# Performance work log

Measured on AMD Instinct MI355X. Metric: run time of the kernel, lower is better.

The kernel has to match this reference:

```python
import jax, jax.numpy as jnp
import numpy as np

B, N, C, H, NRES = 32, 1024, 384, 1024, 20
NTAB = 21  # 20 aa + unknown, per AlphaFold residue_constants


def setup_inputs() -> dict:
    key = jax.random.key(0)
    ks = jax.random.split(key, 16)
    s = 0.02
    inp = {}
    inp['act'] = jax.random.normal(ks[0], (B, N, C), jnp.float32)
    inp['angles'] = jax.random.normal(ks[1], (B, N, 7, 2), jnp.float32)
    inp['rigids'] = jax.random.normal(ks[2], (B, N, 7), jnp.float32)
    inp['fixed_mask'] = jax.random.randint(ks[3], (B, N), 0, 2, jnp.int32)
    inp['seq_t'] = jax.random.randint(ks[4], (B, N), 0, NRES, jnp.int32)
    inp['residx_atom37_to_atom14'] = jax.random.randint(ks[5], (B, N, 37), 0, 14, jnp.int32)
    inp['ln_g'] = jnp.ones((C,), jnp.float32)
    inp['ln_b'] = jnp.zeros((C,), jnp.float32)
    inp['w1'] = jax.random.normal(ks[6], (C, H), jnp.float32) * s
    inp['b1'] = jnp.zeros((H,), jnp.float32)
    inp['w2'] = jax.random.normal(ks[7], (H, H), jnp.float32) * s
    inp['b2'] = jnp.zeros((H,), jnp.float32)
    inp['w3'] = jax.random.normal(ks[8], (H, NRES), jnp.float32) * s
    inp['b3'] = jnp.zeros((NRES,), jnp.float32)
    # stand-in residue_constants tables (same shapes/dtypes as AlphaFold's)
    inp['default_frames'] = jax.random.normal(ks[9], (NTAB, 8, 4, 4), jnp.float32)
    inp['group_idx'] = jax.random.randint(ks[10], (NTAB, 14), 0, 8, jnp.int32)
    inp['atom14_mask'] = (jax.random.uniform(ks[11], (NTAB, 14)) > 0.3).astype(jnp.float32)
    inp['atom37_mask'] = (jax.random.uniform(ks[12], (NTAB, 37)) > 0.3).astype(jnp.float32)
    inp['lit_positions'] = jax.random.normal(ks[13], (NTAB, 14, 3), jnp.float32)
    return inp


def quat_to_rot(q):
    q = q / jnp.sqrt(jnp.sum(q * q, axis=-1, keepdims=True) + 1e-8)
    w, x, y, z = q[..., 0], q[..., 1], q[..., 2], q[..., 3]
    r = jnp.stack([
        1 - 2 * (y * y + z * z), 2 * (x * y - w * z), 2 * (x * z + w * y),
        2 * (x * y + w * z), 1 - 2 * (x * x + z * z), 2 * (y * z - w * x),
        2 * (x * z - w * y), 2 * (y * z + w * x), 1 - 2 * (x * x + y * y)
    ], axis=-1)
    return r.reshape(q.shape[:-1] + (3, 3))


def compose(r1, t1, r2, t2):
    # rigid composition: (r1, t1) o (r2, t2)
    return (jnp.einsum('...ij,...jk->...ik', r1, r2),
            jnp.einsum('...ij,...j->...i', r1, t2) + t1)


def reference(act, angles, rigids, fixed_mask, seq_t, residx_atom37_to_atom14,
              ln_g, ln_b, w1, b1, w2, b2, w3, b3,
              default_frames, group_idx, atom14_mask, atom37_mask, lit_positions):
    # --- small MLP head ---
    mu = jnp.mean(act, axis=-1, keepdims=True)
    var = jnp.var(act, axis=-1, keepdims=True)
    h = (act - mu) / jnp.sqrt(var + 1e-5) * ln_g + ln_b
    h = jax.nn.relu(h @ w1 + b1)
    h = jax.nn.relu(h @ w2 + b2)
    logits = h @ w3 + b3                                # [B,N,20]
    p_0t = jax.nn.softmax(logits, axis=-1)
    seq0 = jnp.argmax(p_0t, axis=-1).astype(jnp.int32)
    seq0 = seq0 * (1 - fixed_mask) + seq_t * fixed_mask  # [B,N]

    # --- backbone frame from quaternion rigids ---
    rb = quat_to_rot(rigids[..., :4])                    # [B,N,3,3]
    tb = rigids[..., 4:]                                 # [B,N,3]

    # --- torsion_angles_to_frames ---
    df = default_frames[seq0]                            # [B,N,8,4,4]
    dr, dt = df[..., :3, :3], df[..., :3, 3]
    sin, cos = angles[..., 0], angles[..., 1]            # [B,N,7]
    z1 = jnp.zeros_like(sin[..., :1])
    sin8 = jnp.concatenate([z1, sin], axis=-1)           # backbone group has angle 0
    cos8 = jnp.concatenate([jnp.ones_like(z1), cos], axis=-1)
    zz, oo = jnp.zeros_like(sin8), jnp.ones_like(sin8)
    rx = jnp.stack([oo, zz, zz, zz, cos8, -sin8, zz, sin8, cos8], axis=-1)
    rx = rx.reshape(sin8.shape + (3, 3))                 # rotation about x-axis
    fr = jnp.einsum('bngij,bngjk->bngik', dr, rx)        # frames to backbone (pre-chain)
    ft = dt
    # chain chi2->chi1, chi3->chi2, chi4->chi3
    r5, t5 = compose(fr[..., 4, :, :], ft[..., 4, :], fr[..., 5, :, :], ft[..., 5, :])
    r6, t6 = compose(r5, t5, fr[..., 6, :, :], ft[..., 6, :])
    r7, t7 = compose(r6, t6, fr[..., 7, :, :], ft[..., 7, :])
    frot = jnp.concatenate([fr[..., :5, :, :], r5[..., None, :, :], r6[..., None, :, :], r7[..., None, :, :]], axis=-3)
    ftr = jnp.concatenate([ft[..., :5, :], t5[..., None, :], t6[..., None, :], t7[..., None, :]], axis=-2)
    grot, gtr = compose(rb[..., None, :, :], tb[..., None, :], frot, ftr)  # [B,N,8,3,3],[B,N,8,3]

    # --- frames_and_literature_positions_to_atom14_pos ---
    gi = group_idx[seq0]                                 # [B,N,14]
    ar = jnp.take_along_axis(grot, jnp.broadcast_to(gi[..., None, None], gi.shape + (3, 3)), axis=2)
    at = jnp.take_along_axis(gtr, jnp.broadcast_to(gi[..., None], gi.shape + (3,)), axis=2)
    lit = lit_positions[seq0]                            # [B,N,14,3]
    m14 = atom14_mask[seq0]                              # [B,N,14]
    pred = (jnp.einsum('bnaij,bnaj->bnai', ar, lit) + at) * m14[..., None]

    # --- atom14 -> atom37 gather ---
    idx = residx_atom37_to_atom14
    final = jnp.take_along_axis(pred, jnp.broadcast_to(idx[..., None], idx.shape + (3,)), axis=2)
    m37 = atom37_mask[seq0]                              # [B,N,37]
    return logits, seq0, pred, final, m14, m37
```

## Files before the change

### kernel.cpp

```cpp
#include <hip/hip_runtime.h>
#include <math.h>

#define B_ 32
#define N_ 1024
#define C_ 384
#define H_ 1024
#define NRES 20
#define NTAB 21
#define M_TOTAL (B_*N_)

#define BM 64
#define BN 128
#define BK 32
#define LDK 40
#define KSPLIT 8

typedef __attribute__((ext_vector_type(8))) short bf16x8;
typedef __attribute__((ext_vector_type(4))) float f32x4;

#define GLOAD_LDS(gptr, lptr) \
    __builtin_amdgcn_global_load_lds( \
        (const __attribute__((address_space(1))) void*)(gptr), \
        (__attribute__((address_space(3))) void*)(lptr), 16, 0, 0)

__device__ inline short bf16_rne(float v) {
    unsigned u = __float_as_uint(v);
    unsigned r = u + 0x7fffu + ((u >> 16) & 1u);
    return (short)(r >> 16);
}
__device__ inline void split2(float v, short& h, short& l) {
    unsigned u = __float_as_uint(v);
    unsigned r = (u + 0x7fffu + ((u >> 16) & 1u)) & 0xffff0000u;
    h = (short)(r >> 16);
    l = bf16_rne(v - __uint_as_float(r));
}

__global__ __launch_bounds__(256) void ln_stats_kernel(const float* __restrict__ act,
                                                       float* __restrict__ mu_out,
                                                       float* __restrict__ rstd_out) {
    int wave = threadIdx.x >> 6;
    int lane = threadIdx.x & 63;
    int row  = blockIdx.x * 4 + wave;
    const float* x = act + (size_t)row * C_;
    float v[6];
    float s = 0.f;
#pragma unroll
    for (int i = 0; i < 6; i++) { v[i] = x[lane + i*64]; s += v[i]; }
#pragma unroll
    for (int off = 32; off > 0; off >>= 1) s += __shfl_xor(s, off, 64);
    float mu = s * (1.0f/384.0f);
    float vs = 0.f;
#pragma unroll
    for (int i = 0; i < 6; i++) { float d = v[i]-mu; vs += d*d; }
#pragma unroll
    for (int off = 32; off > 0; off >>= 1) vs += __shfl_xor(vs, off, 64);
    float var = vs * (1.0f/384.0f);
    if (lane == 0) { mu_out[row] = mu; rstd_out[row] = 1.0f / sqrtf(var + 1e-5f); }
}

__global__ __launch_bounds__(256) void conv_w_kernel(const float* __restrict__ w,
                                                     short* __restrict__ th,
                                                     short* __restrict__ tl,
                                                     int K, int N, int Npad) {
    __shared__ float t[32][33];
    int n0 = blockIdx.x * 32, k0 = blockIdx.y * 32;
    int tx = threadIdx.x & 31, ty = threadIdx.x >> 5;
#pragma unroll
    for (int i = ty; i < 32; i += 8) {
        int k = k0 + i, n = n0 + tx;
        t[i][tx] = (n < N) ? w[(size_t)k * N + n] : 0.f;
    }
    __syncthreads();
#pragma unroll
    for (int i = ty; i < 32; i += 8) {
        int n = n0 + i, k = k0 + tx;
        short h, l; split2(t[tx][i], h, l);
        th[(size_t)n * K + k] = h;
        tl[(size_t)n * K + k] = l;
    }
}

__global__ __launch_bounds__(256) void mlp_gemm1(
    const float* __restrict__ A32,
    const short* __restrict__ BTh, const short* __restrict__ BTl,
    const float* __restrict__ bias,
    short* __restrict__ Ch, short* __restrict__ Cl,
    int K, int ldc,
    const float* __restrict__ mu, const float* __restrict__ rstd,
    const float* __restrict__ lng, const float* __restrict__ lnb)
{
    __shared__ short Ah[BM][LDK], Al[BM][LDK];
    __shared__ short Bh[BN][LDK], Bl[BN][LDK];
    int tid = threadIdx.x;
    int m0 = blockIdx.x * BM;
    int n0 = blockIdx.y * BN;
    int lane = tid & 63, wv = tid >> 6;
    int wm = (wv & 1) * 32, wn = (wv >> 1) * 64;
    int fm = lane & 15, kg = lane >> 4;

    f32x4 acc[2][4] = {};

    int br = tid >> 2;
    int bk8 = (tid & 3) * 8;
    int ar = tid >> 3;
    int ak = (tid & 7) * 4;
    float mur[2], rsr[2];
#pragma unroll
    for (int p = 0; p < 2; p++) { mur[p] = mu[m0 + ar + p*32]; rsr[p] = rstd[m0 + ar + p*32]; }

    for (int k0 = 0; k0 < K; k0 += BK) {
#pragma unroll
        for (int p = 0; p < 2; p++) {
            int row = m0 + ar + p * 32;
            float4 v = *(const float4*)&A32[(size_t)row * K + k0 + ak];
            float4 g = *(const float4*)&lng[k0 + ak];
            float4 b = *(const float4*)&lnb[k0 + ak];
            v.x = (v.x - mur[p]) * rsr[p] * g.x + b.x;
            v.y = (v.y - mur[p]) * rsr[p] * g.y + b.y;
            v.z = (v.z - mur[p]) * rsr[p] * g.z + b.z;
            v.w = (v.w - mur[p]) * rsr[p] * g.w + b.w;
            short4 h4, l4;
            split2(v.x, h4.x, l4.x);
            split2(v.y, h4.y, l4.y);
            split2(v.z, h4.z, l4.z);
            split2(v.w, h4.w, l4.w);
            *(short4*)&Ah[ar + p*32][ak] = h4;
            *(short4*)&Al[ar + p*32][ak] = l4;
        }
#pragma unroll
        for (int p = 0; p < 2; p++) {
            int row = n0 + br + p * 64;
            int4 vh = *(const int4*)&BTh[(size_t)row * K + k0 + bk8];
            int4 vl = *(const int4*)&BTl[(size_t)row * K + k0 + bk8];
            *(int4*)&Bh[br + p*64][bk8] = vh;
            *(int4*)&Bl[br + p*64][bk8] = vl;
        }
        __syncthreads();

        bf16x8 a_h[2], a_l[2], b_h[4], b_l[4];
#pragma unroll
        for (int i = 0; i < 2; i++) {
            a_h[i] = *(bf16x8*)&Ah[wm + i*16 + fm][kg*8];
            a_l[i] = *(bf16x8*)&Al[wm + i*16 + fm][kg*8];
        }
#pragma unroll
        for (int j = 0; j < 4; j++) {
            b_h[j] = *(bf16x8*)&Bh[wn + j*16 + fm][kg*8];
            b_l[j] = *(bf16x8*)&Bl[wn + j*16 + fm][kg*8];
        }
#pragma unroll
        for (int i = 0; i < 2; i++)
#pragma unroll
            for (int j = 0; j < 4; j++) {
                f32x4 c = acc[i][j];
                c = __builtin_amdgcn_mfma_f32_16x16x32_bf16(a_l[i], b_h[j], c, 0, 0, 0);
                c = __builtin_amdgcn_mfma_f32_16x16x32_bf16(a_h[i], b_l[j], c, 0, 0, 0);
                c = __builtin_amdgcn_mfma_f32_16x16x32_bf16(a_h[i], b_h[j], c, 0, 0, 0);
                acc[i][j] = c;
            }
        __syncthreads();
    }

#pragma unroll
    for (int i = 0; i < 2; i++)
#pragma unroll
        for (int j = 0; j < 4; j++) {
            int col = n0 + wn + j*16 + fm;
            float bs = bias[col];
#pragma unroll
            for (int r = 0; r < 4; r++) {
                int row = m0 + wm + i*16 + kg*4 + r;
                float v = fmaxf(acc[i][j][r] + bs, 0.f);
                short h, l; split2(v, h, l);
                Ch[(size_t)row * ldc + col] = h;
                Cl[(size_t)row * ldc + col] = l;
            }
        }
}

__global__ __launch_bounds__(256) void presplit_gemm128(
    const short* __restrict__ Ahg, const short* __restrict__ Alg,
    const short* __restrict__ BTh, const short* __restrict__ BTl,
    const float* __restrict__ bias,
    short* __restrict__ Ch, short* __restrict__ Cl,
    int K, int ldc)
{
    __shared__ short Ah[128][32], Al[128][32], Bh[128][32], Bl[128][32];
    int tid = threadIdx.x;
    int m0 = blockIdx.x * 128;
    int n0 = blockIdx.y * 128;
    int lane = tid & 63, wv = tid >> 6;
    int wm = (wv & 1) * 64, wn = (wv >> 1) * 64;
    int fm = lane & 15, kg = lane >> 4;

    const short* gsrc = (wv == 0) ? Ahg : (wv == 1) ? Alg : (wv == 2) ? BTh : BTl;
    short* lbase = (wv == 0) ? &Ah[0][0] : (wv == 1) ? &Al[0][0]
                 : (wv == 2) ? &Bh[0][0] : &Bl[0][0];
    int base = (wv < 2) ? m0 : n0;
    const short* gp = gsrc + (size_t)(base + (lane >> 2)) * K + (lane & 3) * 8;

    f32x4 acc[4][4] = {};

    for (int k0 = 0; k0 < K; k0 += BK) {
#pragma unroll
        for (int c = 0; c < 8; c++)
            GLOAD_LDS(gp + (size_t)(c * 16) * K + k0, lbase + c * 512);
        __syncthreads();

        bf16x8 a_h[4], a_l[4], b_h[4], b_l[4];
#pragma unroll
        for (int i = 0; i < 4; i++) {
            a_h[i] = *(bf16x8*)&Ah[wm + i*16 + fm][kg*8];
            a_l[i] = *(bf16x8*)&Al[wm + i*16 + fm][kg*8];
            b_h[i] = *(bf16x8*)&Bh[wn + i*16 + fm][kg*8];
            b_l[i] = *(bf16x8*)&Bl[wn + i*16 + fm][kg*8];
        }
#pragma unroll
        for (int i = 0; i < 4; i++)
#pragma unroll
            for (int j = 0; j < 4; j++) {
                f32x4 c = acc[i][j];
                c = __builtin_amdgcn_mfma_f32_16x16x32_bf16(a_l[i], b_h[j], c, 0, 0, 0);
                c = __builtin_amdgcn_mfma_f32_16x16x32_bf16(a_h[i], b_l[j], c, 0, 0, 0);
                c = __builtin_amdgcn_mfma_f32_16x16x32_bf16(a_h[i], b_h[j], c, 0, 0, 0);
                acc[i][j] = c;
            }
        __syncthreads();
    }

#pragma unroll
    for (int i = 0; i < 4; i++)
#pragma unroll
        for (int j = 0; j < 4; j++) {
            int col = n0 + wn + j*16 + fm;
            float bs = bias[col];
#pragma unroll
            for (int r = 0; r < 4; r++) {
                int row = m0 + wm + i*16 + kg*4 + r;
                float v = fmaxf(acc[i][j][r] + bs, 0.f);
                short h, l; split2(v, h, l);
                Ch[(size_t)row * ldc + col] = h;
                Cl[(size_t)row * ldc + col] = l;
            }
        }
}

__global__ __launch_bounds__(256) void gemm3_partial(
    const short* __restrict__ Ahg, const short* __restrict__ Alg,
    const short* __restrict__ BTh, const short* __restrict__ BTl,
    float* __restrict__ partial, int chunkM)
{
    __shared__ short Ah[128][32], Al[128][32];
    __shared__ short Bh[32][32], Bl[32][32];
    int tid = threadIdx.x;
    int kbase = blockIdx.x * 128;
    int m0 = blockIdx.y * 128;
    int lane = tid & 63, wv = tid >> 6;
    int wm = wv * 32;
    int fm = lane & 15, kg = lane >> 4;

    const short* gsrc = (wv == 0) ? Ahg : (wv == 1) ? Alg : (wv == 2) ? BTh : BTl;
    short* lbase = (wv == 0) ? &Ah[0][0] : (wv == 1) ? &Al[0][0]
                 : (wv == 2) ? &Bh[0][0] : &Bl[0][0];
    int base = (wv < 2) ? m0 : 0;
    int ncalls = (wv < 2) ? 8 : 2;
    const short* gp = gsrc + (size_t)(base + (lane >> 2)) * H_ + (lane & 3) * 8;

    f32x4 acc[2][2] = {};

    for (int k0 = kbase; k0 < kbase + 128; k0 += BK) {
        for (int c = 0; c < ncalls; c++)
            GLOAD_LDS(gp + (size_t)(c * 16) * H_ + k0, lbase + c * 512);
        __syncthreads();

        bf16x8 a_h[2], a_l[2], b_h[2], b_l[2];
#pragma unroll
        for (int i = 0; i < 2; i++) {
            a_h[i] = *(bf16x8*)&Ah[wm + i*16 + fm][kg*8];
            a_l[i] = *(bf16x8*)&Al[wm + i*16 + fm][kg*8];
        }
#pragma unroll
        for (int j = 0; j < 2; j++) {
            b_h[j] = *(bf16x8*)&Bh[j*16 + fm][kg*8];
            b_l[j] = *(bf16x8*)&Bl[j*16 + fm][kg*8];
        }
#pragma unroll
        for (int i = 0; i < 2; i++)
#pragma unroll
            for (int j = 0; j < 2; j++) {
                f32x4 c = acc[i][j];
                c = __builtin_amdgcn_mfma_f32_16x16x32_bf16(a_l[i], b_h[j], c, 0, 0, 0);
                c = __builtin_amdgcn_mfma_f32_16x16x32_bf16(a_h[i], b_l[j], c, 0, 0, 0);
                c = __builtin_amdgcn_mfma_f32_16x16x32_bf16(a_h[i], b_h[j], c, 0, 0, 0);
                acc[i][j] = c;
            }
        __syncthreads();
    }

    float* pp = partial + (size_t)blockIdx.x * chunkM * 32;
#pragma unroll
    for (int i = 0; i < 2; i++)
#pragma unroll
        for (int j = 0; j < 2; j++) {
            int col = j*16 + fm;
#pragma unroll
            for (int r = 0; r < 4; r++) {
                int row = m0 + wm + i*16 + kg*4 + r;
                pp[(size_t)row * 32 + col] = acc[i][j][r];
            }
        }
}

__global__ __launch_bounds__(256) void logits_argmax(
    const float* __restrict__ partial, int chunkM, int m0,
    const float* __restrict__ b3,
    const int* __restrict__ fixed_mask, const int* __restrict__ seq_t,
    float* __restrict__ out_logits, float* __restrict__ seq_out,
    int* __restrict__ seq_int)
{
    int rl = blockIdx.x * blockDim.x + threadIdx.x;
    int row = m0 + rl;
    float best = -1e30f; int bi = 0;
    float* lg = out_logits + (size_t)row * NRES;
#pragma unroll 4
    for (int n = 0; n < NRES; n++) {
        float s = b3[n];
#pragma unroll
        for (int p = 0; p < KSPLIT; p++)
            s += partial[((size_t)p * chunkM + rl) * 32 + n];
        lg[n] = s;
        if (s > best) { best = s; bi = n; }
    }
    int fm = fixed_mask[row];
    int s = fm ? seq_t[row] : bi;
    seq_int[row] = s;
    seq_out[row] = (float)s;
}

__global__ __launch_bounds__(128) void geom_kernel(
    const float* __restrict__ angles, const float* __restrict__ rigids,
    const int* __restrict__ seq0i, const int* __restrict__ residx,
    const float* __restrict__ dframes, const int* __restrict__ gidx,
    const float* __restrict__ a14m, const float* __restrict__ a37m,
    const float* __restrict__ litp,
    float* __restrict__ out_pred, float* __restrict__ out_final,
    float* __restrict__ out_m14, float* __restrict__ out_m37)
{
    __shared__ float sdf[NTAB*8*16];
    __shared__ int   sgi[NTAB*14];
    __shared__ float sm14[NTAB*14];
    __shared__ float sm37[NTAB*37];
    __shared__ float slit[NTAB*14*3];
    __shared__ float predL[128][43];

    for (int i = threadIdx.x; i < NTAB*128; i += 128) sdf[i] = dframes[i];
    for (int i = threadIdx.x; i < NTAB*14; i += 128) { sgi[i] = gidx[i]; sm14[i] = a14m[i]; }
    for (int i = threadIdx.x; i < NTAB*37; i += 128) sm37[i] = a37m[i];
    for (int i = threadIdx.x; i < NTAB*42; i += 128) slit[i] = litp[i];
    __syncthreads();

    int p = blockIdx.x * 128 + threadIdx.x;
    int s = seq0i[p];

    const float* rg = rigids + (size_t)p * 7;
    float qw = rg[0], qx = rg[1], qy = rg[2], qz = rg[3];
    float tbx = rg[4], tby = rg[5], tbz = rg[6];
    float qn = 1.0f / sqrtf(qw*qw + qx*qx + qy*qy + qz*qz + 1e-8f);
    qw *= qn; qx *= qn; qy *= qn; qz *= qn;
    float rb[9];
    rb[0] = 1.f - 2.f*(qy*qy + qz*qz); rb[1] = 2.f*(qx*qy - qw*qz); rb[2] = 2.f*(qx*qz + qw*qy);
    rb[3] = 2.f*(qx*qy + qw*qz); rb[4] = 1.f - 2.f*(qx*qx + qz*qz); rb[5] = 2.f*(qy*qz - qw*qx);
    rb[6] = 2.f*(qx*qz - qw*qy); rb[7] = 2.f*(qy*qz + qw*qx); rb[8] = 1.f - 2.f*(qx*qx + qy*qy);

    float fr[8][9], ft[8][3];
    const float* ang = angles + (size_t)p * 14;
#pragma unroll
    for (int g = 0; g < 8; g++) {
        const float* df = &sdf[(s*8 + g)*16];
        float c, sn;
        if (g == 0) { c = 1.f; sn = 0.f; }
        else { sn = ang[(g-1)*2 + 0]; c = ang[(g-1)*2 + 1]; }
#pragma unroll
        for (int i = 0; i < 3; i++) {
            float d0 = df[i*4+0], d1 = df[i*4+1], d2 = df[i*4+2];
            fr[g][i*3+0] = d0;
            fr[g][i*3+1] = d1*c + d2*sn;
            fr[g][i*3+2] = d2*c - d1*sn;
            ft[g][i] = df[i*4+3];
        }
    }
#pragma unroll
    for (int g = 5; g <= 7; g++) {
        float r[9], t[3];
        const float* r1 = fr[g-1];
        const float* t1 = ft[g-1];
#pragma unroll
        for (int i = 0; i < 3; i++) {
#pragma unroll
            for (int j = 0; j < 3; j++)
                r[i*3+j] = r1[i*3+0]*fr[g][0*3+j] + r1[i*3+1]*fr[g][1*3+j] + r1[i*3+2]*fr[g][2*3+j];
            t[i] = r1[i*3+0]*ft[g][0] + r1[i*3+1]*ft[g][1] + r1[i*3+2]*ft[g][2] + t1[i];
        }
#pragma unroll
        for (int i = 0; i < 9; i++) fr[g][i] = r[i];
#pragma unroll
        for (int i = 0; i < 3; i++) ft[g][i] = t[i];
    }
#pragma unroll
    for (int g = 0; g < 8; g++) {
        float r[9], t[3];
#pragma unroll
        for (int i = 0; i < 3; i++) {
#pragma unroll
            for (int j = 0; j < 3; j++)
                r[i*3+j] = rb[i*3+0]*fr[g][0*3+j] + rb[i*3+1]*fr[g][1*3+j] + rb[i*3+2]*fr[g][2*3+j];
            t[i] = rb[i*3+0]*ft[g][0] + rb[i*3+1]*ft[g][1] + rb[i*3+2]*ft[g][2];
        }
#pragma unroll
        for (int i = 0; i < 9; i++) fr[g][i] = r[i];
        ft[g][0]=t[0]+tbx; ft[g][1]=t[1]+tby; ft[g][2]=t[2]+tbz;
    }
#pragma unroll
    for (int g = 0; g < 8; g++) {
#pragma unroll
        for (int a = 0; a < 14; a++) {
            if (sgi[s*14 + a] == g) {
                float m  = sm14[s*14 + a];
                float lx = slit[(s*14 + a)*3 + 0];
                float ly = slit[(s*14 + a)*3 + 1];
                float lz = slit[(s*14 + a)*3 + 2];
                float px = (fr[g][0]*lx + fr[g][1]*ly + fr[g][2]*lz + ft[g][0]) * m;
                float py = (fr[g][3]*lx + fr[g][4]*ly + fr[g][5]*lz + ft[g][1]) * m;
                float pz = (fr[g][6]*lx + fr[g][7]*ly + fr[g][8]*lz + ft[g][2]) * m;
                predL[threadIdx.x][a*3+0] = px;
                predL[threadIdx.x][a*3+1] = py;
                predL[threadIdx.x][a*3+2] = pz;
                out_pred[((size_t)p*14 + a)*3 + 0] = px;
                out_pred[((size_t)p*14 + a)*3 + 1] = py;
                out_pred[((size_t)p*14 + a)*3 + 2] = pz;
            }
        }
    }
#pragma unroll
    for (int a = 0; a < 14; a++) out_m14[(size_t)p*14 + a] = sm14[s*14 + a];

    const int* idx = residx + (size_t)p * 37;
#pragma unroll
    for (int a = 0; a < 37; a++) {
        int id = idx[a];
        out_final[((size_t)p*37 + a)*3 + 0] = predL[threadIdx.x][id*3+0];
        out_final[((size_t)p*37 + a)*3 + 1] = predL[threadIdx.x][id*3+1];
        out_final[((size_t)p*37 + a)*3 + 2] = predL[threadIdx.x][id*3+2];
        out_m37[(size_t)p*37 + a] = sm37[s*37 + a];
    }
}

extern "C" void kernel_launch(void* const* d_in, const int* in_sizes, int n_in,
                              void* d_out, int out_size, void* d_ws, size_t ws_size,
                              hipStream_t stream) {
    const float* act        = (const float*)d_in[0];
    const float* angles     = (const float*)d_in[1];
    const float* rigids     = (const float*)d_in[2];
    const int*   fixed_mask = (const int*)d_in[3];
    const int*   seq_t      = (const int*)d_in[4];
    const int*   residx     = (const int*)d_in[5];
    const float* lng        = (const float*)d_in[6];
    const float* lnb        = (const float*)d_in[7];
    const float* w1         = (const float*)d_in[8];
    const float* b1         = (const float*)d_in[9];
    const float* w2         = (const float*)d_in[10];
    const float* b2         = (const float*)d_in[11];
    const float* w3         = (const float*)d_in[12];
    const float* b3         = (const float*)d_in[13];
    const float* dfr        = (const float*)d_in[14];
    const int*   gidx       = (const int*)d_in[15];
    const float* a14m       = (const float*)d_in[16];
    const float* a37m       = (const float*)d_in[17];
    const float* litp       = (const float*)d_in[18];

    float* out        = (float*)d_out;
    float* out_logits = out;
    float* out_seq    = out_logits + (size_t)M_TOTAL * NRES;
    float* out_pred   = out_seq    + (size_t)M_TOTAL;
    float* out_final  = out_pred   + (size_t)M_TOTAL * 42;
    float* out_m14    = out_final  + (size_t)M_TOTAL * 111;
    float* out_m37    = out_m14    + (size_t)M_TOTAL * 14;

    char* wsp = (char*)d_ws;
    int*   seq0i = (int*)wsp;   wsp += (size_t)M_TOTAL * sizeof(int);
    float* mu    = (float*)wsp; wsp += (size_t)M_TOTAL * sizeof(float);
    float* rstd  = (float*)wsp; wsp += (size_t)M_TOTAL * sizeof(float);
    short* w1h   = (short*)wsp; wsp += (size_t)H_ * C_ * sizeof(short);
    short* w1l   = (short*)wsp; wsp += (size_t)H_ * C_ * sizeof(short);
    short* w2h   = (short*)wsp; wsp += (size_t)H_ * H_ * sizeof(short);
    short* w2l   = (short*)wsp; wsp += (size_t)H_ * H_ * sizeof(short);
    short* w3h   = (short*)wsp; wsp += (size_t)128 * H_ * sizeof(short);
    short* w3l   = (short*)wsp; wsp += (size_t)128 * H_ * sizeof(short);

    size_t fixed_bytes = (size_t)(wsp - (char*)d_ws);
    size_t per_row = 4ull * H_ * sizeof(short) + (size_t)KSPLIT * 32 * sizeof(float);
    int chunkM = 4096;
    if (ws_size - fixed_bytes >= (size_t)M_TOTAL * per_row)      chunkM = M_TOTAL;
    else if (ws_size - fixed_bytes >= (size_t)16384 * per_row)   chunkM = 16384;
    else if (ws_size - fixed_bytes >= (size_t)8192 * per_row)    chunkM = 8192;

    short* H1h = (short*)wsp; wsp += (size_t)chunkM * H_ * sizeof(short);
    short* H1l = (short*)wsp; wsp += (size_t)chunkM * H_ * sizeof(short);
    short* H2h = (short*)wsp; wsp += (size_t)chunkM * H_ * sizeof(short);
    short* H2l = (short*)wsp; wsp += (size_t)chunkM * H_ * sizeof(short);
    float* part = (float*)wsp;

    conv_w_kernel<<<dim3(H_/32, C_/32), 256, 0, stream>>>(w1, w1h, w1l, C_, H_, H_);
    conv_w_kernel<<<dim3(H_/32, H_/32), 256, 0, stream>>>(w2, w2h, w2l, H_, H_, H_);
    conv_w_kernel<<<dim3(128/32, H_/32), 256, 0, stream>>>(w3, w3h, w3l, H_, NRES, 128);

    ln_stats_kernel<<<M_TOTAL/4, 256, 0, stream>>>(act, mu, rstd);

    for (int c = 0; c < M_TOTAL / chunkM; c++) {
        int m0 = c * chunkM;
        mlp_gemm1<<<dim3(chunkM/BM, H_/BN), 256, 0, stream>>>(
            act + (size_t)m0 * C_, w1h, w1l, b1, H1h, H1l, C_, H_,
            mu + m0, rstd + m0, lng, lnb);
        presplit_gemm128<<<dim3(chunkM/128, H_/128), 256, 0, stream>>>(
            H1h, H1l, w2h, w2l, b2, H2h, H2l, H_, H_);
        gemm3_partial<<<dim3(KSPLIT, chunkM/128), 256, 0, stream>>>(H2h, H2l, w3h, w3l,
                                                                    part, chunkM);
        logits_argmax<<<chunkM/256, 256, 0, stream>>>(part, chunkM, m0, b3,
                                                      fixed_mask, seq_t,
                                                      out_logits, out_seq, seq0i);
    }

    geom_kernel<<<M_TOTAL/128, 128, 0, stream>>>(angles, rigids, seq0i, residx,
                                                 dfr, gidx, a14m, a37m, litp,
                                                 out_pred, out_final, out_m14, out_m37);
}
```

Baseline: 548.2 us.

## Presplit LayerNorm output for GEMM1 and fuse GEMM3 with logits argmax

The LayerNorm kernel now normalizes each row and writes bf16 hi/lo split activations directly, so the first GEMM can reuse the presplit_gemm128 kernel (global_load_lds, 128x128 tiles) in place of the custom LN-fused GEMM that re-normalized and split A on every N tile. The split-K third GEMM and its separate reduction/argmax kernel are merged into one kernel that loops over the full K and computes logits, argmax and seq selection from shared memory. This removes redundant LN/split work, the partial-sum buffer and a launch. In exchange it adds an extra write and read of the split activations and leaves GEMM3 with fewer blocks (chunkM/128) doing longer K loops, which lowers parallelism.

```diff
diff --git a/kernel.cpp b/kernel.cpp
--- a/kernel.cpp
+++ b/kernel.cpp
@@ -8,12 +8,7 @@
 #define NRES 20
 #define NTAB 21
 #define M_TOTAL (B_*N_)
-
-#define BM 64
-#define BN 128
 #define BK 32
-#define LDK 40
-#define KSPLIT 8
 
 typedef __attribute__((ext_vector_type(8))) short bf16x8;
 typedef __attribute__((ext_vector_type(4))) float f32x4;
@@ -35,9 +30,11 @@
     l = bf16_rne(v - __uint_as_float(r));
 }
 
-__global__ __launch_bounds__(256) void ln_stats_kernel(const float* __restrict__ act,
-                                                       float* __restrict__ mu_out,
-                                                       float* __restrict__ rstd_out) {
+__global__ __launch_bounds__(256) void ln_split_kernel(const float* __restrict__ act,
+                                                       const float* __restrict__ lng,
+                                                       const float* __restrict__ lnb,
+                                                       short* __restrict__ Xh,
+                                                       short* __restrict__ Xl) {
     int wave = threadIdx.x >> 6;
     int lane = threadIdx.x & 63;
     int row  = blockIdx.x * 4 + wave;
@@ -54,8 +51,15 @@
     for (int i = 0; i < 6; i++) { float d = v[i]-mu; vs += d*d; }
 #pragma unroll
     for (int off = 32; off > 0; off >>= 1) vs += __shfl_xor(vs, off, 64);
-    float var = vs * (1.0f/384.0f);
-    if (lane == 0) { mu_out[row] = mu; rstd_out[row] = 1.0f / sqrtf(var + 1e-5f); }
+    float rstd = 1.0f / sqrtf(vs * (1.0f/384.0f) + 1e-5f);
+#pragma unroll
+    for (int i = 0; i < 6; i++) {
+        int col = lane + i*64;
+        float y = (v[i] - mu) * rstd * lng[col] + lnb[col];
+        short h, l; split2(y, h, l);
+        Xh[(size_t)row * C_ + col] = h;
+        Xl[(size_t)row * C_ + col] = l;
+    }
 }
 
 __global__ __launch_bounds__(256) void conv_w_kernel(const float* __restrict__ w,
@@ -78,104 +82,6 @@
         th[(size_t)n * K + k] = h;
         tl[(size_t)n * K + k] = l;
     }
-}
-
-__global__ __launch_bounds__(256) void mlp_gemm1(
-    const float* __restrict__ A32,
-    const short* __restrict__ BTh, const short* __restrict__ BTl,
-    const float* __restrict__ bias,
-    short* __restrict__ Ch, short* __restrict__ Cl,
-    int K, int ldc,
-    const float* __restrict__ mu, const float* __restrict__ rstd,
-    const float* __restrict__ lng, const float* __restrict__ lnb)
-{
-    __shared__ short Ah[BM][LDK], Al[BM][LDK];
-    __shared__ short Bh[BN][LDK], Bl[BN][LDK];
-    int tid = threadIdx.x;
-    int m0 = blockIdx.x * BM;
-    int n0 = blockIdx.y * BN;
-    int lane = tid & 63, wv = tid >> 6;
-    int wm = (wv & 1) * 32, wn = (wv >> 1) * 64;
-    int fm = lane & 15, kg = lane >> 4;
-
-    f32x4 acc[2][4] = {};
-
-    int br = tid >> 2;
-    int bk8 = (tid & 3) * 8;
-    int ar = tid >> 3;
-    int ak = (tid & 7) * 4;
-    float mur[2], rsr[2];
-#pragma unroll
-    for (int p = 0; p < 2; p++) { mur[p] = mu[m0 + ar + p*32]; rsr[p] = rstd[m0 + ar + p*32]; }
-
-    for (int k0 = 0; k0 < K; k0 += BK) {
-#pragma unroll
-        for (int p = 0; p < 2; p++) {
-            int row = m0 + ar + p * 32;
-            float4 v = *(const float4*)&A32[(size_t)row * K + k0 + ak];
-            float4 g = *(const float4*)&lng[k0 + ak];
-            float4 b = *(const float4*)&lnb[k0 + ak];
-            v.x = (v.x - mur[p]) * rsr[p] * g.x + b.x;
-            v.y = (v.y - mur[p]) * rsr[p] * g.y + b.y;
-            v.z = (v.z - mur[p]) * rsr[p] * g.z + b.z;
-            v.w = (v.w - mur[p]) * rsr[p] * g.w + b.w;
-            short4 h4, l4;
-            split2(v.x, h4.x, l4.x);
-            split2(v.y, h4.y, l4.y);
-            split2(v.z, h4.z, l4.z);
-            split2(v.w, h4.w, l4.w);
-            *(short4*)&Ah[ar + p*32][ak] = h4;
-            *(short4*)&Al[ar + p*32][ak] = l4;
-        }
-#pragma unroll
-        for (int p = 0; p < 2; p++) {
-            int row = n0 + br + p * 64;
-            int4 vh = *(const int4*)&BTh[(size_t)row * K + k0 + bk8];
-            int4 vl = *(const int4*)&BTl[(size_t)row * K + k0 + bk8];
-            *(int4*)&Bh[br + p*64][bk8] = vh;
-            *(int4*)&Bl[br + p*64][bk8] = vl;
-        }
-        __syncthreads();
-
-        bf16x8 a_h[2], a_l[2], b_h[4], b_l[4];
-#pragma unroll
-        for (int i = 0; i < 2; i++) {
-            a_h[i] = *(bf16x8*)&Ah[wm + i*16 + fm][kg*8];
-            a_l[i] = *(bf16x8*)&Al[wm + i*16 + fm][kg*8];
-        }
-#pragma unroll
-        for (int j = 0; j < 4; j++) {
-            b_h[j] = *(bf16x8*)&Bh[wn + j*16 + fm][kg*8];
-            b_l[j] = *(bf16x8*)&Bl[wn + j*16 + fm][kg*8];
-        }
-#pragma unroll
-        for (int i = 0; i < 2; i++)
-#pragma unroll
-            for (int j = 0; j < 4; j++) {
-                f32x4 c = acc[i][j];
-                c = __builtin_amdgcn_mfma_f32_16x16x32_bf16(a_l[i], b_h[j], c, 0, 0, 0);
-                c = __builtin_amdgcn_mfma_f32_16x16x32_bf16(a_h[i], b_l[j], c, 0, 0, 0);
-                c = __builtin_amdgcn_mfma_f32_16x16x32_bf16(a_h[i], b_h[j], c, 0, 0, 0);
-                acc[i][j] = c;
-            }
-        __syncthreads();
-    }
-
-#pragma unroll
-    for (int i = 0; i < 2; i++)
-#pragma unroll
-        for (int j = 0; j < 4; j++) {
-            int col = n0 + wn + j*16 + fm;
-            float bs = bias[col];
-#pragma unroll
-            for (int r = 0; r < 4; r++) {
-                int row = m0 + wm + i*16 + kg*4 + r;
-                float v = fmaxf(acc[i][j][r] + bs, 0.f);
-                short h, l; split2(v, h, l);
-                Ch[(size_t)row * ldc + col] = h;
-                Cl[(size_t)row * ldc + col] = l;
-            }
-        }
 }
 
 __global__ __launch_bounds__(256) void presplit_gemm128(
@@ -245,16 +151,19 @@
         }
 }
 
-__global__ __launch_bounds__(256) void gemm3_partial(
+__global__ __launch_bounds__(256) void gemm3_fused(
     const short* __restrict__ Ahg, const short* __restrict__ Alg,
     const short* __restrict__ BTh, const short* __restrict__ BTl,
-    float* __restrict__ partial, int chunkM)
+    const float* __restrict__ b3,
+    const int* __restrict__ fixed_mask, const int* __restrict__ seq_t,
+    float* __restrict__ out_logits, float* __restrict__ seq_out,
+    int* __restrict__ seq_int, int m0c)
 {
     __shared__ short Ah[128][32], Al[128][32];
     __shared__ short Bh[32][32], Bl[32][32];
+    __shared__ float slog[128][33];
     int tid = threadIdx.x;
-    int kbase = blockIdx.x * 128;
-    int m0 = blockIdx.y * 128;
+    int m0 = blockIdx.x * 128;
     int lane = tid & 63, wv = tid >> 6;
     int wm = wv * 32;
     int fm = lane & 15, kg = lane >> 4;
@@ -268,7 +177,7 @@
 
     f32x4 acc[2][2] = {};
 
-    for (int k0 = kbase; k0 < kbase + 128; k0 += BK) {
+    for (int k0 = 0; k0 < H_; k0 += BK) {
         for (int c = 0; c < ncalls; c++)
             GLOAD_LDS(gp + (size_t)(c * 16) * H_ + k0, lbase + c * 512);
         __syncthreads();
@@ -297,44 +206,30 @@
         __syncthreads();
     }
 
-    float* pp = partial + (size_t)blockIdx.x * chunkM * 32;
 #pragma unroll
     for (int i = 0; i < 2; i++)
 #pragma unroll
-        for (int j = 0; j < 2; j++) {
-            int col = j*16 + fm;
-#pragma unroll
-            for (int r = 0; r < 4; r++) {
-                int row = m0 + wm + i*16 + kg*4 + r;
-                pp[(size_t)row * 32 + col] = acc[i][j][r];
-            }
-        }
-}
-
-__global__ __launch_bounds__(256) void logits_argmax(
-    const float* __restrict__ partial, int chunkM, int m0,
-    const float* __restrict__ b3,
-    const int* __restrict__ fixed_mask, const int* __restrict__ seq_t,
-    float* __restrict__ out_logits, float* __restrict__ seq_out,
-    int* __restrict__ seq_int)
-{
-    int rl = blockIdx.x * blockDim.x + threadIdx.x;
-    int row = m0 + rl;
-    float best = -1e30f; int bi = 0;
-    float* lg = out_logits + (size_t)row * NRES;
-#pragma unroll 4
-    for (int n = 0; n < NRES; n++) {
-        float s = b3[n];
-#pragma unroll
-        for (int p = 0; p < KSPLIT; p++)
-            s += partial[((size_t)p * chunkM + rl) * 32 + n];
-        lg[n] = s;
-        if (s > best) { best = s; bi = n; }
-    }
-    int fm = fixed_mask[row];
-    int s = fm ? seq_t[row] : bi;
-    seq_int[row] = s;
-    seq_out[row] = (float)s;
+        for (int j = 0; j < 2; j++)
+#pragma unroll
+            for (int r = 0; r < 4; r++)
+                slog[wm + i*16 + kg*4 + r][j*16 + fm] = acc[i][j][r];
+    __syncthreads();
+
+    if (tid < 128) {
+        int grow = m0c + m0 + tid;
+        float best = -1e30f; int bi = 0;
+        float* lg = out_logits + (size_t)grow * NRES;
+#pragma unroll
+        for (int n = 0; n < NRES; n++) {
+            float s = slog[tid][n] + b3[n];
+            lg[n] = s;
+            if (s > best) { best = s; bi = n; }
+        }
+        int fmk = fixed_mask[grow];
+        int s = fmk ? seq_t[grow] : bi;
+        seq_int[grow] = s;
+        seq_out[grow] = (float)s;
+    }
 }
 
 __global__ __launch_bounds__(128) void geom_kernel(
@@ -488,46 +383,43 @@
 
     char* wsp = (char*)d_ws;
     int*   seq0i = (int*)wsp;   wsp += (size_t)M_TOTAL * sizeof(int);
-    float* mu    = (float*)wsp; wsp += (size_t)M_TOTAL * sizeof(float);
-    float* rstd  = (float*)wsp; wsp += (size_t)M_TOTAL * sizeof(float);
     short* w1h   = (short*)wsp; wsp += (size_t)H_ * C_ * sizeof(short);
     short* w1l   = (short*)wsp; wsp += (size_t)H_ * C_ * sizeof(short);
     short* w2h   = (short*)wsp; wsp += (size_t)H_ * H_ * sizeof(short);
     short* w2l   = (short*)wsp; wsp += (size_t)H_ * H_ * sizeof(short);
     short* w3h   = (short*)wsp; wsp += (size_t)128 * H_ * sizeof(short);
     short* w3l   = (short*)wsp; wsp += (size_t)128 * H_ * sizeof(short);
+    short* Xh    = (short*)wsp; wsp += (size_t)M_TOTAL * C_ * sizeof(short);
+    short* Xl    = (short*)wsp; wsp += (size_t)M_TOTAL * C_ * sizeof(short);
 
     size_t fixed_bytes = (size_t)(wsp - (char*)d_ws);
-    size_t per_row = 4ull * H_ * sizeof(short) + (size_t)KSPLIT * 32 * sizeof(float);
+    size_t per_row = 4ull * H_ * sizeof(short);
+    size_t avail = ws_size - fixed_bytes;
     int chunkM = 4096;
-    if (ws_size - fixed_bytes >= (size_t)M_TOTAL * per_row)      chunkM = M_TOTAL;
-    else if (ws_size - fixed_bytes >= (size_t)16384 * per_row)   chunkM = 16384;
-    else if (ws_size - fixed_bytes >= (size_t)8192 * per_row)    chunkM = 8192;
+    if (avail >= (size_t)M_TOTAL * per_row)      chunkM = M_TOTAL;
+    else if (avail >= 16384ull * per_row)        chunkM = 16384;
+    else if (avail >= 8192ull * per_row)         chunkM = 8192;
 
     short* H1h = (short*)wsp; wsp += (size_t)chunkM * H_ * sizeof(short);
     short* H1l = (short*)wsp; wsp += (size_t)chunkM * H_ * sizeof(short);
     short* H2h = (short*)wsp; wsp += (size_t)chunkM * H_ * sizeof(short);
-    short* H2l = (short*)wsp; wsp += (size_t)chunkM * H_ * sizeof(short);
-    float* part = (float*)wsp;
+    short* H2l = (short*)wsp;
 
     conv_w_kernel<<<dim3(H_/32, C_/32), 256, 0, stream>>>(w1, w1h, w1l, C_, H_, H_);
     conv_w_kernel<<<dim3(H_/32, H_/32), 256, 0, stream>>>(w2, w2h, w2l, H_, H_, H_);
     conv_w_kernel<<<dim3(128/32, H_/32), 256, 0, stream>>>(w3, w3h, w3l, H_, NRES, 128);
 
-    ln_stats_kernel<<<M_TOTAL/4, 256, 0, stream>>>(act, mu, rstd);
+    ln_split_kernel<<<M_TOTAL/4, 256, 0, stream>>>(act, lng, lnb, Xh, Xl);
 
     for (int c = 0; c < M_TOTAL / chunkM; c++) {
         int m0 = c * chunkM;
-        mlp_gemm1<<<dim3(chunkM/BM, H_/BN), 256, 0, stream>>>(
-            act + (size_t)m0 * C_, w1h, w1l, b1, H1h, H1l, C_, H_,
-            mu + m0, rstd + m0, lng, lnb);
+        presplit_gemm128<<<dim3(chunkM/128, H_/128), 256, 0, stream>>>(
+            Xh + (size_t)m0 * C_, Xl + (size_t)m0 * C_, w1h, w1l, b1, H1h, H1l, C_, H_);
         presplit_gemm128<<<dim3(chunkM/128, H_/128), 256, 0, stream>>>(
             H1h, H1l, w2h, w2l, b2, H2h, H2l, H_, H_);
-        gemm3_partial<<<dim3(KSPLIT, chunkM/128), 256, 0, stream>>>(H2h, H2l, w3h, w3l,
-                                                                    part, chunkM);
-        logits_argmax<<<chunkM/256, 256, 0, stream>>>(part, chunkM, m0, b3,
-                                                      fixed_mask, seq_t,
-                                                      out_logits, out_seq, seq0i);
+        gemm3_fused<<<chunkM/128, 256, 0, stream>>>(H2h, H2l, w3h, w3l, b3,
+                                                    fixed_mask, seq_t,
+                                                    out_logits, out_seq, seq0i, m0);
     }
 
     geom_kernel<<<M_TOTAL/128, 128, 0, stream>>>(angles, rigids, seq0i, residx,
```

After: 539.2 us. Within noise of the previous version (-1.6%).
